# Performance work log

Measured on AMD Instinct MI355X. Metric: run time of the kernel, lower is better.

## Reference

```python
import jax, jax.numpy as jnp
import numpy as np

DIM = 256
HEADS = 8
WS = 7          # window_size
WN = 8          # window_num per side
H = W = WS * WN # 56
B = 32
MLP_HIDDEN = 4 * DIM
SCALE = (DIM // HEADS) ** -0.5
LN_EPS = 1e-5


def _rel_index(ws):
    # pairwise relative position index inside a ws x ws window (dense 0..(2ws-1)^2-1,
    # so remap_position_index is the identity relabeling)
    ch, cw = np.meshgrid(np.arange(ws), np.arange(ws), indexing='ij')
    cf = np.stack([ch.ravel(), cw.ravel()])            # (2, ws*ws)
    rel = cf[:, :, None] - cf[:, None, :]              # (2, N, N)
    rel = rel.transpose(1, 2, 0).astype(np.int32)
    rel[..., 0] += ws - 1
    rel[..., 1] += ws - 1
    rel[..., 0] *= 2 * ws - 1
    return rel.sum(-1)                                 # (N, N) in [0, (2ws-1)^2)


def _layernorm(x, g, b):
    m = x.mean(-1, keepdims=True)
    v = ((x - m) ** 2).mean(-1, keepdims=True)
    return (x - m) * jax.lax.rsqrt(v + LN_EPS) * g + b


def _mhsa(x, qkv_w, qkv_b, proj_w, proj_b, bias):
    # x: (B_, N, C); bias: (nH, N, N) or None
    B_, N, C = x.shape
    hd = C // HEADS
    qkv = (x @ qkv_w.T + qkv_b).reshape(B_, N, 3, HEADS, hd).transpose(2, 0, 3, 1, 4)
    q, k, v = qkv[0], qkv[1], qkv[2]
    attn = jnp.einsum('bhqd,bhkd->bhqk', q * SCALE, k)
    if bias is not None:
        attn = attn + bias[None]
    attn = jax.nn.softmax(attn, axis=-1)
    out = jnp.einsum('bhqk,bhkd->bhqd', attn, v).transpose(0, 2, 1, 3).reshape(B_, N, C)
    return out @ proj_w.T + proj_b


def setup_inputs() -> dict:
    key = jax.random.key(0)
    ks = jax.random.split(key, 8)
    f32 = jnp.float32
    return {
        'regional_tokens': jax.random.normal(ks[0], (B, WN * WN, DIM), f32),
        'x': jax.random.normal(ks[1], (B, H * W, DIM), f32),
        'norm1_g': jnp.ones((DIM,), f32), 'norm1_b': jnp.zeros((DIM,), f32),
        'norm2_g': jnp.ones((DIM,), f32), 'norm2_b': jnp.zeros((DIM,), f32),
        'norm3_g': jnp.ones((DIM,), f32), 'norm3_b': jnp.zeros((DIM,), f32),
        'qkv_w': jax.random.normal(ks[2], (3 * DIM, DIM), f32) * 0.02,
        'qkv_b': jnp.zeros((3 * DIM,), f32),
        'proj_w': jax.random.normal(ks[3], (DIM, DIM), f32) * 0.02,
        'proj_b': jnp.zeros((DIM,), f32),
        'bias_table': jax.random.normal(ks[4], ((2 * WS - 1) ** 2, HEADS), f32) * 0.02,
        'fc1_w': jax.random.normal(ks[5], (MLP_HIDDEN, DIM), f32) * 0.02,
        'fc1_b': jnp.zeros((MLP_HIDDEN,), f32),
        'fc2_w': jax.random.normal(ks[6], (DIM, MLP_HIDDEN), f32) * 0.02,
        'fc2_b': jnp.zeros((DIM,), f32),
        'rel_index': jnp.asarray(_rel_index(WS)),
    }


def reference(regional_tokens, x, norm1_g, norm1_b, norm2_g, norm2_b, norm3_g, norm3_b,
              qkv_w, qkv_b, proj_w, proj_b, bias_table, fc1_w, fc1_b, fc2_w, fc2_b,
              rel_index):
    Bb, L, C = x.shape
    nW = regional_tokens.shape[1]
    ws2 = WS * WS
    # --- RSA: attention over regional tokens (no relative bias) ---
    regional_tokens = regional_tokens + _mhsa(
        _layernorm(regional_tokens, norm1_g, norm1_b), qkv_w, qkv_b, proj_w, proj_b, None)
    # --- window partition of x: (B,H,W,C) -> (nW*B, ws*ws, C) (batch-major) ---
    xw = x.reshape(Bb, H // WS, WS, W // WS, WS, C)
    xw = xw.transpose(0, 1, 3, 2, 4, 5).reshape(-1, ws2, C)
    # regional tokens reshaped window-major, exactly as the torch code does
    reg = regional_tokens.transpose(1, 0, 2).reshape(nW * Bb, 1, C)
    t = jnp.concatenate([reg, xw], axis=1)  # (nW*B, 1+ws2, C)
    # --- LSA relative position bias, zero-padded for the regional token ---
    bias = bias_table[rel_index]                       # (ws2, ws2, nH)
    bias = jnp.pad(bias, ((1, 0), (1, 0), (0, 0)))      # (1+ws2, 1+ws2, nH)
    bias = bias.transpose(2, 0, 1)                      # (nH, N, N)
    t = t + _mhsa(_layernorm(t, norm2_g, norm2_b), qkv_w, qkv_b, proj_w, proj_b, bias)
    # --- MLP ---
    h = _layernorm(t, norm3_g, norm3_b)
    h = jax.nn.gelu(h @ fc1_w.T + fc1_b, approximate=False) @ fc2_w.T + fc2_b
    t = t + h
    # --- split back ---
    reg_out = t[:, 0, :].reshape(nW, Bb, C).transpose(1, 0, 2)   # (B, nW, C)
    xw = t[:, 1:, :].reshape(Bb, H // WS, W // WS, WS, WS, C)
    x_out = xw.transpose(0, 1, 3, 2, 4, 5).reshape(Bb, L, C)
    return reg_out, x_out
```

## Files before the change

kernel.cpp:

```cpp
#include <hip/hip_runtime.h>
#include <math.h>

#define SCALE_Q 0.17677669529663687f

typedef __attribute__((ext_vector_type(8))) short bf16x8;
typedef __attribute__((ext_vector_type(4))) float f32x4;
typedef __attribute__((ext_vector_type(4))) unsigned short u16x4;

static __device__ __forceinline__ unsigned short f2bf(float f) {
    unsigned int u = __float_as_uint(f);
    u += 0x7FFF + ((u >> 16) & 1);
    return (unsigned short)(u >> 16);
}

static __device__ __forceinline__ float gelu_fast(float v) {
    float s = v * (0.7978845608f + 0.0356774081f * v * v);
    float e = __expf(-2.0f * s);
    return v * __builtin_amdgcn_rcpf(1.0f + e);
}

static __device__ __forceinline__ void barrier_lds_only() {
    asm volatile("s_waitcnt lgkmcnt(0)" ::: "memory");
    __builtin_amdgcn_s_barrier();
    asm volatile("" ::: "memory");
}

__global__ void prep_kernel(const float* __restrict__ qkv_w, const float* __restrict__ proj_w,
                            const float* __restrict__ fc1_w, const float* __restrict__ fc2_w,
                            const float* __restrict__ bias_table, const int* __restrict__ rel_index,
                            unsigned short* __restrict__ wq, unsigned short* __restrict__ wp,
                            unsigned short* __restrict__ w1, unsigned short* __restrict__ w2,
                            float* __restrict__ bias_pad) {
    int tid = blockIdx.x * blockDim.x + threadIdx.x;
    int stride = gridDim.x * blockDim.x;
    for (int i = tid; i < 768 * 256; i += stride) wq[i] = f2bf(qkv_w[i]);
    for (int i = tid; i < 256 * 256; i += stride) wp[i] = f2bf(proj_w[i]);
    for (int i = tid; i < 1024 * 256; i += stride) w1[i] = f2bf(fc1_w[i]);
    for (int i = tid; i < 256 * 1024; i += stride) w2[i] = f2bf(fc2_w[i]);
    for (int i = tid; i < 8 * 64 * 64; i += stride) {
        int h = i >> 12, q = (i >> 6) & 63, k = i & 63;
        float v;
        if (k >= 50) v = -1e30f;
        else if (q == 0 || k == 0 || q >= 50) v = 0.f;
        else v = bias_table[rel_index[(q - 1) * 49 + (k - 1)] * 8 + h];
        bias_pad[i] = v;
    }
}

template <int IS_RSA>
__global__ __launch_bounds__(1024, 4) void attn_kernel(
    const float* __restrict__ reg_tok, const float* __restrict__ x,
    const float* __restrict__ reg2_in, float* __restrict__ out,
    const float* __restrict__ ln_g, const float* __restrict__ ln_b,
    const unsigned short* __restrict__ wq, const float* __restrict__ qkv_b,
    const unsigned short* __restrict__ wp, const float* __restrict__ proj_b,
    const float* __restrict__ bias_pad) {
    __shared__ __align__(16) unsigned char smem[140288];
    unsigned short* regA = (unsigned short*)smem;
    unsigned short* regB = (unsigned short*)(smem + 36864);
    unsigned short* vT   = (unsigned short*)(smem + 103424);

    const int tid = threadIdx.x;
    const int lane = tid & 63;
    const int wid = tid >> 6;
    const int widu = __builtin_amdgcn_readfirstlane(wid);
    const int l15 = lane & 15;
    const int lg = lane >> 4;
    const int u = blockIdx.x;
    const int NV = IS_RSA ? 64 : 50;
    const f32x4 fzero = {0.f, 0.f, 0.f, 0.f};

    int reg_off = 0, xb = 0, wi = 0, wj = 0;
    if (!IS_RSA) {
        reg_off = ((u & 31) * 64 + (u >> 5)) * 256;
        xb = u >> 6;
        int xn = u & 63;
        wi = xn >> 3; wj = xn & 7;
    }

    for (int r = wid; r < 64; r += 16) {
        if (r < NV) {
            const float* src;
            if (IS_RSA) src = reg_tok + (u * 64 + r) * 256;
            else if (r == 0) src = reg2_in + reg_off;
            else {
                int p = r - 1;
                src = x + (xb * 3136 + (wi * 7 + p / 7) * 56 + (wj * 7 + p % 7)) * 256;
            }
            f32x4 v = *(const f32x4*)(src + lane * 4);
            float s = v[0] + v[1] + v[2] + v[3];
            float s2 = v[0] * v[0] + v[1] * v[1] + v[2] * v[2] + v[3] * v[3];
            #pragma unroll
            for (int m = 1; m < 64; m <<= 1) { s += __shfl_xor(s, m); s2 += __shfl_xor(s2, m); }
            float mean = s * 0.00390625f;
            float rstd = rsqrtf(s2 * 0.00390625f - mean * mean + 1e-5f);
            u16x4 o;
            #pragma unroll
            for (int j = 0; j < 4; ++j) {
                int c = lane * 4 + j;
                o[j] = f2bf((v[j] - mean) * rstd * ln_g[c] + ln_b[c]);
            }
            *(u16x4*)(regA + r * 264 + lane * 4) = o;
        } else {
            u16x4 z = {0, 0, 0, 0};
            *(u16x4*)(regA + r * 264 + lane * 4) = z;
        }
    }
    barrier_lds_only();

    const int h = wid >> 1;
    const int qb = (wid & 1) * 32;

    bf16x8 wpf[8];
    {
        f32x4 acc[4][3];
        #pragma unroll
        for (int mi = 0; mi < 4; ++mi)
            #pragma unroll
            for (int t = 0; t < 3; ++t) acc[mi][t] = fzero;
        #pragma unroll
        for (int ks = 0; ks < 8; ++ks) {
            int k = ks * 32 + lg * 8;
            bf16x8 a[4], b[3];
            #pragma unroll
            for (int mi = 0; mi < 4; ++mi) a[mi] = *(const bf16x8*)(regA + (mi * 16 + l15) * 264 + k);
            #pragma unroll
            for (int t = 0; t < 3; ++t) b[t] = *(const bf16x8*)(wq + (wid * 48 + t * 16 + l15) * 256 + k);
            #pragma unroll
            for (int mi = 0; mi < 4; ++mi)
                #pragma unroll
                for (int t = 0; t < 3; ++t)
                    acc[mi][t] = __builtin_amdgcn_mfma_f32_16x16x32_bf16(a[mi], b[t], acc[mi][t], 0, 0, 0);
        }
        #pragma unroll
        for (int ks = 0; ks < 8; ++ks)
            wpf[ks] = *(const bf16x8*)(wp + (wid * 16 + l15) * 256 + ks * 32 + lg * 8);
        #pragma unroll
        for (int t = 0; t < 3; ++t) {
            if (3 * widu + t < 32) {
                #pragma unroll
                for (int mi = 0; mi < 4; ++mi) {
                    int col = wid * 48 + t * 16 + l15;
                    float bias = qkv_b[col];
                    #pragma unroll
                    for (int r = 0; r < 4; ++r) {
                        int row = mi * 16 + lg * 4 + r;
                        regB[row * 520 + col] = f2bf(acc[mi][t][r] + bias);
                    }
                }
            } else {
                #pragma unroll
                for (int mi = 0; mi < 4; ++mi) {
                    int col = wid * 48 + t * 16 + l15;
                    float bias = qkv_b[col];
                    #pragma unroll
                    for (int r = 0; r < 4; ++r) {
                        int row = mi * 16 + lg * 4 + r;
                        vT[(col - 512) * 72 + row] = f2bf(acc[mi][t][r] + bias);
                    }
                }
            }
        }
    }

    f32x4 bv[4][2];
    if (!IS_RSA) {
        #pragma unroll
        for (int mi = 0; mi < 4; ++mi)
            #pragma unroll
            for (int nj = 0; nj < 2; ++nj)
                bv[mi][nj] = *(const f32x4*)(bias_pad + h * 4096 + (qb + nj * 16 + l15) * 64 + mi * 16 + lg * 4);
    }
    barrier_lds_only();

    f32x4 st[4][2];
    {
        int k0 = h * 32 + lg * 8;
        bf16x8 af[4], bfq[2];
        #pragma unroll
        for (int mi = 0; mi < 4; ++mi) af[mi] = *(const bf16x8*)(regB + (mi * 16 + l15) * 520 + 256 + k0);
        #pragma unroll
        for (int nj = 0; nj < 2; ++nj) bfq[nj] = *(const bf16x8*)(regB + (qb + nj * 16 + l15) * 520 + k0);
        #pragma unroll
        for (int mi = 0; mi < 4; ++mi)
            #pragma unroll
            for (int nj = 0; nj < 2; ++nj)
                st[mi][nj] = __builtin_amdgcn_mfma_f32_16x16x32_bf16(af[mi], bfq[nj], fzero, 0, 0, 0);
    }

    u16x4 pf[4][2];
    #pragma unroll
    for (int nj = 0; nj < 2; ++nj) {
        float ps[4][4];
        float mx = -3.0e38f;
        #pragma unroll
        for (int mi = 0; mi < 4; ++mi)
            #pragma unroll
            for (int r = 0; r < 4; ++r) {
                float t = st[mi][nj][r] * SCALE_Q;
                if (!IS_RSA) t += bv[mi][nj][r];
                ps[mi][r] = t;
                mx = fmaxf(mx, t);
            }
        mx = fmaxf(mx, __shfl_xor(mx, 16));
        mx = fmaxf(mx, __shfl_xor(mx, 32));
        float sum = 0.f;
        #pragma unroll
        for (int mi = 0; mi < 4; ++mi)
            #pragma unroll
            for (int r = 0; r < 4; ++r) { ps[mi][r] = __expf(ps[mi][r] - mx); sum += ps[mi][r]; }
        sum += __shfl_xor(sum, 16);
        sum += __shfl_xor(sum, 32);
        float inv = __builtin_amdgcn_rcpf(sum);
        #pragma unroll
        for (int mi = 0; mi < 4; ++mi) {
            u16x4 p4;
            #pragma unroll
            for (int r = 0; r < 4; ++r) p4[r] = f2bf(ps[mi][r] * inv);
            pf[mi][nj] = p4;
        }
    }

    f32x4 ov[2][2];
    #pragma unroll
    for (int m2 = 0; m2 < 2; ++m2) { ov[m2][0] = fzero; ov[m2][1] = fzero; }
    #pragma unroll
    for (int kt = 0; kt < 4; ++kt) {
        bf16x8 pb[2];
        #pragma unroll
        for (int nj = 0; nj < 2; ++nj) {
            bf16x8 t;
            t[0] = (short)pf[kt][nj][0]; t[1] = (short)pf[kt][nj][1];
            t[2] = (short)pf[kt][nj][2]; t[3] = (short)pf[kt][nj][3];
            t[4] = 0; t[5] = 0; t[6] = 0; t[7] = 0;
            pb[nj] = t;
        }
        #pragma unroll
        for (int m2 = 0; m2 < 2; ++m2) {
            u16x4 av = *(const u16x4*)(vT + (h * 32 + m2 * 16 + l15) * 72 + kt * 16 + lg * 4);
            bf16x8 a8;
            a8[0] = (short)av[0]; a8[1] = (short)av[1]; a8[2] = (short)av[2]; a8[3] = (short)av[3];
            a8[4] = 0; a8[5] = 0; a8[6] = 0; a8[7] = 0;
            #pragma unroll
            for (int nj = 0; nj < 2; ++nj)
                ov[m2][nj] = __builtin_amdgcn_mfma_f32_16x16x32_bf16(a8, pb[nj], ov[m2][nj], 0, 0, 0);
        }
    }
    #pragma unroll
    for (int m2 = 0; m2 < 2; ++m2)
        #pragma unroll
        for (int nj = 0; nj < 2; ++nj) {
            u16x4 o4;
            #pragma unroll
            for (int r = 0; r < 4; ++r) o4[r] = f2bf(ov[m2][nj][r]);
            *(u16x4*)(regA + (qb + nj * 16 + l15) * 264 + h * 32 + m2 * 16 + lg * 4) = o4;
        }
    barrier_lds_only();

    {
        f32x4 acc[4];
        #pragma unroll
        for (int mi = 0; mi < 4; ++mi) acc[mi] = fzero;
        #pragma unroll
        for (int ks = 0; ks < 8; ++ks) {
            int k = ks * 32 + lg * 8;
            bf16x8 a[4];
            #pragma unroll
            for (int mi = 0; mi < 4; ++mi) a[mi] = *(const bf16x8*)(regA + (mi * 16 + l15) * 264 + k);
            #pragma unroll
            for (int mi = 0; mi < 4; ++mi)
                acc[mi] = __builtin_amdgcn_mfma_f32_16x16x32_bf16(a[mi], wpf[ks], acc[mi], 0, 0, 0);
        }
        int col = wid * 16 + l15;
        float pb = proj_b[col];
        #pragma unroll
        for (int mi = 0; mi < 4; ++mi)
            #pragma unroll
            for (int r = 0; r < 4; ++r) {
                int row = mi * 16 + lg * 4 + r;
                if (row < NV) {
                    float val = acc[mi][r] + pb;
                    if (IS_RSA) {
                        int off = (u * 64 + row) * 256 + col;
                        out[off] = val + reg_tok[off];
                    } else if (row == 0) {
                        out[reg_off + col] = val + reg2_in[reg_off + col];
                    } else {
                        int p = row - 1;
                        int off = (xb * 3136 + (wi * 7 + p / 7) * 56 + (wj * 7 + p % 7)) * 256 + col;
                        out[524288 + off] = val + x[off];
                    }
                }
            }
    }
}

__global__ __launch_bounds__(512, 4) void mlp_kernel(
    float* __restrict__ dout,
    const float* __restrict__ ln_g, const float* __restrict__ ln_b,
    const unsigned short* __restrict__ w1, const float* __restrict__ b1,
    const unsigned short* __restrict__ w2, const float* __restrict__ b2) {
    __shared__ __align__(16) unsigned short xst[64 * 264];
    __shared__ __align__(16) unsigned short hld[2][64 * 136];
    const int tid = threadIdx.x;
    const int lane = tid & 63;
    const int wid = tid >> 6;
    const int l15 = lane & 15;
    const int lg = lane >> 4;
    const int row0 = blockIdx.x * 64;
    const f32x4 fzero = {0.f, 0.f, 0.f, 0.f};

    #pragma unroll
    for (int i = 0; i < 8; ++i) {
        int r = wid * 8 + i;
        f32x4 v = *(const f32x4*)(dout + (row0 + r) * 256 + lane * 4);
        float s = v[0] + v[1] + v[2] + v[3];
        float s2 = v[0] * v[0] + v[1] * v[1] + v[2] * v[2] + v[3] * v[3];
        #pragma unroll
        for (int m = 1; m < 64; m <<= 1) { s += __shfl_xor(s, m); s2 += __shfl_xor(s2, m); }
        float mean = s * 0.00390625f;
        float rstd = rsqrtf(s2 * 0.00390625f - mean * mean + 1e-5f);
        u16x4 o;
        #pragma unroll
        for (int j = 0; j < 4; ++j) {
            int c = lane * 4 + j;
            o[j] = f2bf((v[j] - mean) * rstd * ln_g[c] + ln_b[c]);
        }
        *(u16x4*)(xst + r * 264 + lane * 4) = o;
    }

    bf16x8 w1f[8];
    #pragma unroll
    for (int ks = 0; ks < 8; ++ks)
        w1f[ks] = *(const bf16x8*)(w1 + (wid * 16 + l15) * 256 + ks * 32 + lg * 8);
    barrier_lds_only();

    f32x4 acc2[4][2];
    #pragma unroll
    for (int mi = 0; mi < 4; ++mi) { acc2[mi][0] = fzero; acc2[mi][1] = fzero; }

    #pragma unroll
    for (int c = 0; c < 8; ++c) {
        unsigned short* hb = &hld[c & 1][0];
        f32x4 acc1[4];
        #pragma unroll
        for (int mi = 0; mi < 4; ++mi) acc1[mi] = fzero;
        #pragma unroll
        for (int ks = 0; ks < 8; ++ks) {
            int k = ks * 32 + lg * 8;
            bf16x8 a[4];
            #pragma unroll
            for (int mi = 0; mi < 4; ++mi)
                a[mi] = *(const bf16x8*)(xst + (mi * 16 + l15) * 264 + k);
            #pragma unroll
            for (int mi = 0; mi < 4; ++mi)
                acc1[mi] = __builtin_amdgcn_mfma_f32_16x16x32_bf16(a[mi], w1f[ks], acc1[mi], 0, 0, 0);
        }
        if (c < 7) {
            #pragma unroll
            for (int ks = 0; ks < 8; ++ks)
                w1f[ks] = *(const bf16x8*)(w1 + ((c + 1) * 128 + wid * 16 + l15) * 256 + ks * 32 + lg * 8);
        }
        {
            int hc = wid * 16 + l15;
            float bb = b1[c * 128 + hc];
            #pragma unroll
            for (int mi = 0; mi < 4; ++mi)
                #pragma unroll
                for (int r = 0; r < 4; ++r)
                    hb[(mi * 16 + lg * 4 + r) * 136 + hc] = f2bf(gelu_fast(acc1[mi][r] + bb));
        }
        bf16x8 w2f[8];
        #pragma unroll
        for (int ks = 0; ks < 4; ++ks)
            #pragma unroll
            for (int ni = 0; ni < 2; ++ni)
                w2f[ks * 2 + ni] = *(const bf16x8*)(w2 + (wid * 32 + ni * 16 + l15) * 1024 + c * 128 + ks * 32 + lg * 8);
        barrier_lds_only();
        #pragma unroll
        for (int ks = 0; ks < 4; ++ks) {
            int k = ks * 32 + lg * 8;
            bf16x8 a[4];
            #pragma unroll
            for (int mi = 0; mi < 4; ++mi)
                a[mi] = *(const bf16x8*)(hb + (mi * 16 + l15) * 136 + k);
            #pragma unroll
            for (int mi = 0; mi < 4; ++mi)
                #pragma unroll
                for (int ni = 0; ni < 2; ++ni)
                    acc2[mi][ni] = __builtin_amdgcn_mfma_f32_16x16x32_bf16(a[mi], w2f[ks * 2 + ni], acc2[mi][ni], 0, 0, 0);
        }
    }
    #pragma unroll
    for (int mi = 0; mi < 4; ++mi)
        #pragma unroll
        for (int ni = 0; ni < 2; ++ni) {
            int col = wid * 32 + ni * 16 + l15;
            float bb = b2[col];
            #pragma unroll
            for (int r = 0; r < 4; ++r) {
                int row = row0 + mi * 16 + lg * 4 + r;
                float* dst = dout + row * 256 + col;
                *dst = acc2[mi][ni][r] + bb + *dst;
            }
        }
}

extern "C" void kernel_launch(void* const* d_in, const int* in_sizes, int n_in,
                              void* d_out, int out_size, void* d_ws, size_t ws_size,
                              hipStream_t stream) {
    const float* regional = (const float*)d_in[0];
    const float* x = (const float*)d_in[1];
    const float* n1g = (const float*)d_in[2];
    const float* n1b = (const float*)d_in[3];
    const float* n2g = (const float*)d_in[4];
    const float* n2b = (const float*)d_in[5];
    const float* n3g = (const float*)d_in[6];
    const float* n3b = (const float*)d_in[7];
    const float* qkvw = (const float*)d_in[8];
    const float* qkvb = (const float*)d_in[9];
    const float* projw = (const float*)d_in[10];
    const float* projb = (const float*)d_in[11];
    const float* btab = (const float*)d_in[12];
    const float* f1w = (const float*)d_in[13];
    const float* f1b = (const float*)d_in[14];
    const float* f2w = (const float*)d_in[15];
    const float* f2b = (const float*)d_in[16];
    const int* relidx = (const int*)d_in[17];

    unsigned char* ws = (unsigned char*)d_ws;
    unsigned short* wq = (unsigned short*)(ws);
    unsigned short* wp = (unsigned short*)(ws + 393216);
    unsigned short* w1 = (unsigned short*)(ws + 524288);
    unsigned short* w2 = (unsigned short*)(ws + 1048576);
    float* bias_pad    = (float*)(ws + 1572864);
    float* reg2        = (float*)(ws + 1703936);

    float* out = (float*)d_out;

    prep_kernel<<<512, 256, 0, stream>>>(qkvw, projw, f1w, f2w, btab, relidx, wq, wp, w1, w2, bias_pad);
    attn_kernel<1><<<32, 1024, 0, stream>>>(regional, x, nullptr, reg2, n1g, n1b, wq, qkvb, wp, projb, nullptr);
    attn_kernel<0><<<2048, 1024, 0, stream>>>(regional, x, reg2, out, n2g, n2b, wq, qkvb, wp, projb, bias_pad);
    mlp_kernel<<<1600, 512, 0, stream>>>(out, n3g, n3b, w1, f1b, w2, f2b);
}
```

Measured before the change: 498.4 us.

## Split fused MLP into separate FC1 and FC2 kernels over row chunks

Replaces the single fused MLP kernel, which kept the hidden activation in LDS, with an FC1+GELU kernel that writes a bf16 hidden buffer to workspace and an FC2 kernel that reads it back and adds the residual. The work runs in four row chunks so the hidden buffer stays small and may stay cache-resident. The aim is better MFMA tiling and occupancy in each GEMM, paid for with extra global traffic for the hidden tensor, eight launches instead of one, and LayerNorm being recomputed for each of the two column halves.

```diff
diff --git a/kernel.cpp b/kernel.cpp
--- a/kernel.cpp
+++ b/kernel.cpp
@@ -295,13 +295,11 @@
     }
 }
 
-__global__ __launch_bounds__(512, 4) void mlp_kernel(
-    float* __restrict__ dout,
-    const float* __restrict__ ln_g, const float* __restrict__ ln_b,
-    const unsigned short* __restrict__ w1, const float* __restrict__ b1,
-    const unsigned short* __restrict__ w2, const float* __restrict__ b2) {
+__global__ __launch_bounds__(512, 4) void fc1_kernel(
+    const float* __restrict__ tin, const float* __restrict__ ln_g,
+    const float* __restrict__ ln_b, const unsigned short* __restrict__ w1,
+    const float* __restrict__ b1, unsigned short* __restrict__ H) {
     __shared__ __align__(16) unsigned short xst[64 * 264];
-    __shared__ __align__(16) unsigned short hld[2][64 * 136];
     const int tid = threadIdx.x;
     const int lane = tid & 63;
     const int wid = tid >> 6;
@@ -313,7 +311,7 @@
     #pragma unroll
     for (int i = 0; i < 8; ++i) {
         int r = wid * 8 + i;
-        f32x4 v = *(const f32x4*)(dout + (row0 + r) * 256 + lane * 4);
+        f32x4 v = *(const f32x4*)(tin + (row0 + r) * 256 + lane * 4);
         float s = v[0] + v[1] + v[2] + v[3];
         float s2 = v[0] * v[0] + v[1] * v[1] + v[2] * v[2] + v[3] * v[3];
         #pragma unroll
@@ -328,82 +326,82 @@
         }
         *(u16x4*)(xst + r * 264 + lane * 4) = o;
     }
-
-    bf16x8 w1f[8];
-    #pragma unroll
-    for (int ks = 0; ks < 8; ++ks)
-        w1f[ks] = *(const bf16x8*)(w1 + (wid * 16 + l15) * 256 + ks * 32 + lg * 8);
-    barrier_lds_only();
-
-    f32x4 acc2[4][2];
-    #pragma unroll
-    for (int mi = 0; mi < 4; ++mi) { acc2[mi][0] = fzero; acc2[mi][1] = fzero; }
-
-    #pragma unroll
-    for (int c = 0; c < 8; ++c) {
-        unsigned short* hb = &hld[c & 1][0];
-        f32x4 acc1[4];
-        #pragma unroll
-        for (int mi = 0; mi < 4; ++mi) acc1[mi] = fzero;
-        #pragma unroll
-        for (int ks = 0; ks < 8; ++ks) {
-            int k = ks * 32 + lg * 8;
-            bf16x8 a[4];
-            #pragma unroll
-            for (int mi = 0; mi < 4; ++mi)
-                a[mi] = *(const bf16x8*)(xst + (mi * 16 + l15) * 264 + k);
-            #pragma unroll
-            for (int mi = 0; mi < 4; ++mi)
-                acc1[mi] = __builtin_amdgcn_mfma_f32_16x16x32_bf16(a[mi], w1f[ks], acc1[mi], 0, 0, 0);
-        }
-        if (c < 7) {
-            #pragma unroll
-            for (int ks = 0; ks < 8; ++ks)
-                w1f[ks] = *(const bf16x8*)(w1 + ((c + 1) * 128 + wid * 16 + l15) * 256 + ks * 32 + lg * 8);
-        }
-        {
-            int hc = wid * 16 + l15;
-            float bb = b1[c * 128 + hc];
-            #pragma unroll
-            for (int mi = 0; mi < 4; ++mi)
-                #pragma unroll
-                for (int r = 0; r < 4; ++r)
-                    hb[(mi * 16 + lg * 4 + r) * 136 + hc] = f2bf(gelu_fast(acc1[mi][r] + bb));
-        }
-        bf16x8 w2f[8];
-        #pragma unroll
-        for (int ks = 0; ks < 4; ++ks)
-            #pragma unroll
-            for (int ni = 0; ni < 2; ++ni)
-                w2f[ks * 2 + ni] = *(const bf16x8*)(w2 + (wid * 32 + ni * 16 + l15) * 1024 + c * 128 + ks * 32 + lg * 8);
-        barrier_lds_only();
-        #pragma unroll
-        for (int ks = 0; ks < 4; ++ks) {
-            int k = ks * 32 + lg * 8;
-            bf16x8 a[4];
-            #pragma unroll
-            for (int mi = 0; mi < 4; ++mi)
-                a[mi] = *(const bf16x8*)(hb + (mi * 16 + l15) * 136 + k);
-            #pragma unroll
-            for (int mi = 0; mi < 4; ++mi)
-                #pragma unroll
-                for (int ni = 0; ni < 2; ++ni)
-                    acc2[mi][ni] = __builtin_amdgcn_mfma_f32_16x16x32_bf16(a[mi], w2f[ks * 2 + ni], acc2[mi][ni], 0, 0, 0);
-        }
-    }
+    __syncthreads();
+
+    const int colbase = blockIdx.y * 512 + wid * 64;
+    f32x4 acc[4][4];
     #pragma unroll
     for (int mi = 0; mi < 4; ++mi)
         #pragma unroll
-        for (int ni = 0; ni < 2; ++ni) {
-            int col = wid * 32 + ni * 16 + l15;
-            float bb = b2[col];
+        for (int ni = 0; ni < 4; ++ni) acc[mi][ni] = fzero;
+    #pragma unroll
+    for (int ks = 0; ks < 8; ++ks) {
+        int k = ks * 32 + lg * 8;
+        bf16x8 a[4], b[4];
+        #pragma unroll
+        for (int mi = 0; mi < 4; ++mi)
+            a[mi] = *(const bf16x8*)(xst + (mi * 16 + l15) * 264 + k);
+        #pragma unroll
+        for (int ni = 0; ni < 4; ++ni)
+            b[ni] = *(const bf16x8*)(w1 + (colbase + ni * 16 + l15) * 256 + k);
+        #pragma unroll
+        for (int mi = 0; mi < 4; ++mi)
+            #pragma unroll
+            for (int ni = 0; ni < 4; ++ni)
+                acc[mi][ni] = __builtin_amdgcn_mfma_f32_16x16x32_bf16(a[mi], b[ni], acc[mi][ni], 0, 0, 0);
+    }
+    #pragma unroll
+    for (int mi = 0; mi < 4; ++mi)
+        #pragma unroll
+        for (int ni = 0; ni < 4; ++ni) {
+            int col = colbase + ni * 16 + l15;
+            float bb = b1[col];
             #pragma unroll
             for (int r = 0; r < 4; ++r) {
                 int row = row0 + mi * 16 + lg * 4 + r;
-                float* dst = dout + row * 256 + col;
-                *dst = acc2[mi][ni][r] + bb + *dst;
-            }
-        }
+                H[row * 1024 + col] = f2bf(gelu_fast(acc[mi][ni][r] + bb));
+            }
+        }
+}
+
+__global__ __launch_bounds__(512, 6) void fc2_kernel(
+    const unsigned short* __restrict__ H, const unsigned short* __restrict__ w2,
+    const float* __restrict__ b2, float* __restrict__ dout) {
+    const int tid = threadIdx.x;
+    const int lane = tid & 63;
+    const int wid = tid >> 6;
+    const int l15 = lane & 15;
+    const int lg = lane >> 4;
+    const int wr = wid >> 1;
+    const int wc = wid & 1;
+    const int rowb = blockIdx.x * 64 + wr * 16;
+    const int colb = blockIdx.y * 128 + wc * 64;
+    const f32x4 fzero = {0.f, 0.f, 0.f, 0.f};
+
+    f32x4 acc[4];
+    #pragma unroll
+    for (int ni = 0; ni < 4; ++ni) acc[ni] = fzero;
+    #pragma unroll
+    for (int ks = 0; ks < 32; ++ks) {
+        int k = ks * 32 + lg * 8;
+        bf16x8 a = *(const bf16x8*)(H + (rowb + l15) * 1024 + k);
+        #pragma unroll
+        for (int ni = 0; ni < 4; ++ni) {
+            bf16x8 b = *(const bf16x8*)(w2 + (colb + ni * 16 + l15) * 1024 + k);
+            acc[ni] = __builtin_amdgcn_mfma_f32_16x16x32_bf16(a, b, acc[ni], 0, 0, 0);
+        }
+    }
+    #pragma unroll
+    for (int ni = 0; ni < 4; ++ni) {
+        int col = colb + ni * 16 + l15;
+        float bb = b2[col];
+        #pragma unroll
+        for (int r = 0; r < 4; ++r) {
+            int row = rowb + lg * 4 + r;
+            float* dst = dout + row * 256 + col;
+            *dst = acc[ni][r] + bb + *dst;
+        }
+    }
 }
 
 extern "C" void kernel_launch(void* const* d_in, const int* in_sizes, int n_in,
@@ -435,11 +433,16 @@
     unsigned short* w2 = (unsigned short*)(ws + 1048576);
     float* bias_pad    = (float*)(ws + 1572864);
     float* reg2        = (float*)(ws + 1703936);
+    unsigned short* Hb = (unsigned short*)(ws + 3801088);
 
     float* out = (float*)d_out;
 
     prep_kernel<<<512, 256, 0, stream>>>(qkvw, projw, f1w, f2w, btab, relidx, wq, wp, w1, w2, bias_pad);
     attn_kernel<1><<<32, 1024, 0, stream>>>(regional, x, nullptr, reg2, n1g, n1b, wq, qkvb, wp, projb, nullptr);
     attn_kernel<0><<<2048, 1024, 0, stream>>>(regional, x, reg2, out, n2g, n2b, wq, qkvb, wp, projb, bias_pad);
-    mlp_kernel<<<1600, 512, 0, stream>>>(out, n3g, n3b, w1, f1b, w2, f2b);
-}
+    for (int c = 0; c < 4; ++c) {
+        float* tc = out + (size_t)c * 25600 * 256;
+        fc1_kernel<<<dim3(400, 2), 512, 0, stream>>>(tc, n3g, n3b, w1, f1b, Hb);
+        fc2_kernel<<<dim3(400, 2), 512, 0, stream>>>(Hb, w2, f2b, tc);
+    }
+}
```

After: 1.040 ms. 2.09x slower.

## Restructure attention kernel to one head per wave with register-resident Q/K/V

Applied to the files above, without the earlier changes.

The attention kernel moves from 1024 threads (two waves per head, each owning half the queries) to 512 threads with one wave per head covering all 64 queries. Each wave computes its own K, Q and V head slices with MFMA and keeps them in registers as zero-padded bf16 fragments, so the large LDS staging buffers for QKV and the transposed V go away. LDS per block shrinks to a single 64x264 bf16 tile, which should allow more resident blocks and cut LDS traffic. In exchange there are fewer waves per block, more registers per wave, and the projection weights are now streamed from global memory inside the k loop instead of being preloaded.

```diff
diff --git a/kernel.cpp b/kernel.cpp
--- a/kernel.cpp
+++ b/kernel.cpp
@@ -48,26 +48,23 @@
 }
 
 template <int IS_RSA>
-__global__ __launch_bounds__(1024, 4) void attn_kernel(
+__global__ __launch_bounds__(512, 4) void attn_kernel(
     const float* __restrict__ reg_tok, const float* __restrict__ x,
     const float* __restrict__ reg2_in, float* __restrict__ out,
     const float* __restrict__ ln_g, const float* __restrict__ ln_b,
     const unsigned short* __restrict__ wq, const float* __restrict__ qkv_b,
     const unsigned short* __restrict__ wp, const float* __restrict__ proj_b,
     const float* __restrict__ bias_pad) {
-    __shared__ __align__(16) unsigned char smem[140288];
-    unsigned short* regA = (unsigned short*)smem;
-    unsigned short* regB = (unsigned short*)(smem + 36864);
-    unsigned short* vT   = (unsigned short*)(smem + 103424);
+    __shared__ __align__(16) unsigned short xln[64 * 264];
 
     const int tid = threadIdx.x;
     const int lane = tid & 63;
     const int wid = tid >> 6;
-    const int widu = __builtin_amdgcn_readfirstlane(wid);
     const int l15 = lane & 15;
     const int lg = lane >> 4;
     const int u = blockIdx.x;
     const int NV = IS_RSA ? 64 : 50;
+    const int h = wid;
     const f32x4 fzero = {0.f, 0.f, 0.f, 0.f};
 
     int reg_off = 0, xb = 0, wi = 0, wj = 0;
@@ -78,7 +75,9 @@
         wi = xn >> 3; wj = xn & 7;
     }
 
-    for (int r = wid; r < 64; r += 16) {
+    #pragma unroll
+    for (int i = 0; i < 8; ++i) {
+        int r = i * 8 + wid;
         if (r < NV) {
             const float* src;
             if (IS_RSA) src = reg_tok + (u * 64 + r) * 256;
@@ -100,108 +99,99 @@
                 int c = lane * 4 + j;
                 o[j] = f2bf((v[j] - mean) * rstd * ln_g[c] + ln_b[c]);
             }
-            *(u16x4*)(regA + r * 264 + lane * 4) = o;
+            *(u16x4*)(xln + r * 264 + lane * 4) = o;
         } else {
             u16x4 z = {0, 0, 0, 0};
-            *(u16x4*)(regA + r * 264 + lane * 4) = z;
-        }
-    }
-    barrier_lds_only();
-
-    const int h = wid >> 1;
-    const int qb = (wid & 1) * 32;
-
-    bf16x8 wpf[8];
+            *(u16x4*)(xln + r * 264 + lane * 4) = z;
+        }
+    }
+    __syncthreads();
+
+    bf16x8 a16k[2][4];
     {
-        f32x4 acc[4][3];
+        f32x4 Kc[2][4];
+        #pragma unroll
+        for (int dc = 0; dc < 2; ++dc)
+            #pragma unroll
+            for (int nt = 0; nt < 4; ++nt) Kc[dc][nt] = fzero;
+        #pragma unroll
+        for (int ks = 0; ks < 8; ++ks) {
+            int k = ks * 32 + lg * 8;
+            bf16x8 aw[2], bx[4];
+            #pragma unroll
+            for (int dc = 0; dc < 2; ++dc)
+                aw[dc] = *(const bf16x8*)(wq + (256 + h * 32 + dc * 16 + l15) * 256 + k);
+            #pragma unroll
+            for (int nt = 0; nt < 4; ++nt)
+                bx[nt] = *(const bf16x8*)(xln + (nt * 16 + l15) * 264 + k);
+            #pragma unroll
+            for (int dc = 0; dc < 2; ++dc)
+                #pragma unroll
+                for (int nt = 0; nt < 4; ++nt)
+                    Kc[dc][nt] = __builtin_amdgcn_mfma_f32_16x16x32_bf16(aw[dc], bx[nt], Kc[dc][nt], 0, 0, 0);
+        }
+        #pragma unroll
+        for (int dc = 0; dc < 2; ++dc) {
+            f32x4 bk = *(const f32x4*)(qkv_b + 256 + h * 32 + dc * 16 + lg * 4);
+            #pragma unroll
+            for (int nt = 0; nt < 4; ++nt) {
+                bf16x8 t;
+                #pragma unroll
+                for (int j = 0; j < 4; ++j) t[j] = (short)f2bf(Kc[dc][nt][j] + bk[j]);
+                t[4] = 0; t[5] = 0; t[6] = 0; t[7] = 0;
+                a16k[dc][nt] = t;
+            }
+        }
+    }
+
+    u16x4 pf[4][4];
+    #pragma unroll
+    for (int nj = 0; nj < 4; ++nj) {
+        f32x4 Qc[2] = {fzero, fzero};
+        #pragma unroll
+        for (int ks = 0; ks < 8; ++ks) {
+            int k = ks * 32 + lg * 8;
+            bf16x8 aw[2];
+            #pragma unroll
+            for (int dc = 0; dc < 2; ++dc)
+                aw[dc] = *(const bf16x8*)(wq + (h * 32 + dc * 16 + l15) * 256 + k);
+            bf16x8 bq = *(const bf16x8*)(xln + (nj * 16 + l15) * 264 + k);
+            #pragma unroll
+            for (int dc = 0; dc < 2; ++dc)
+                Qc[dc] = __builtin_amdgcn_mfma_f32_16x16x32_bf16(aw[dc], bq, Qc[dc], 0, 0, 0);
+        }
+        bf16x8 b16[2];
+        #pragma unroll
+        for (int dc = 0; dc < 2; ++dc) {
+            f32x4 bq = *(const f32x4*)(qkv_b + h * 32 + dc * 16 + lg * 4);
+            bf16x8 t;
+            #pragma unroll
+            for (int j = 0; j < 4; ++j) t[j] = (short)f2bf(Qc[dc][j] + bq[j]);
+            t[4] = 0; t[5] = 0; t[6] = 0; t[7] = 0;
+            b16[dc] = t;
+        }
+        f32x4 st[4];
+        #pragma unroll
+        for (int mi = 0; mi < 4; ++mi) st[mi] = fzero;
         #pragma unroll
         for (int mi = 0; mi < 4; ++mi)
             #pragma unroll
-            for (int t = 0; t < 3; ++t) acc[mi][t] = fzero;
-        #pragma unroll
-        for (int ks = 0; ks < 8; ++ks) {
-            int k = ks * 32 + lg * 8;
-            bf16x8 a[4], b[3];
-            #pragma unroll
-            for (int mi = 0; mi < 4; ++mi) a[mi] = *(const bf16x8*)(regA + (mi * 16 + l15) * 264 + k);
-            #pragma unroll
-            for (int t = 0; t < 3; ++t) b[t] = *(const bf16x8*)(wq + (wid * 48 + t * 16 + l15) * 256 + k);
-            #pragma unroll
-            for (int mi = 0; mi < 4; ++mi)
-                #pragma unroll
-                for (int t = 0; t < 3; ++t)
-                    acc[mi][t] = __builtin_amdgcn_mfma_f32_16x16x32_bf16(a[mi], b[t], acc[mi][t], 0, 0, 0);
-        }
-        #pragma unroll
-        for (int ks = 0; ks < 8; ++ks)
-            wpf[ks] = *(const bf16x8*)(wp + (wid * 16 + l15) * 256 + ks * 32 + lg * 8);
-        #pragma unroll
-        for (int t = 0; t < 3; ++t) {
-            if (3 * widu + t < 32) {
-                #pragma unroll
-                for (int mi = 0; mi < 4; ++mi) {
-                    int col = wid * 48 + t * 16 + l15;
-                    float bias = qkv_b[col];
-                    #pragma unroll
-                    for (int r = 0; r < 4; ++r) {
-                        int row = mi * 16 + lg * 4 + r;
-                        regB[row * 520 + col] = f2bf(acc[mi][t][r] + bias);
-                    }
-                }
-            } else {
-                #pragma unroll
-                for (int mi = 0; mi < 4; ++mi) {
-                    int col = wid * 48 + t * 16 + l15;
-                    float bias = qkv_b[col];
-                    #pragma unroll
-                    for (int r = 0; r < 4; ++r) {
-                        int row = mi * 16 + lg * 4 + r;
-                        vT[(col - 512) * 72 + row] = f2bf(acc[mi][t][r] + bias);
-                    }
-                }
-            }
-        }
-    }
-
-    f32x4 bv[4][2];
-    if (!IS_RSA) {
-        #pragma unroll
-        for (int mi = 0; mi < 4; ++mi)
-            #pragma unroll
-            for (int nj = 0; nj < 2; ++nj)
-                bv[mi][nj] = *(const f32x4*)(bias_pad + h * 4096 + (qb + nj * 16 + l15) * 64 + mi * 16 + lg * 4);
-    }
-    barrier_lds_only();
-
-    f32x4 st[4][2];
-    {
-        int k0 = h * 32 + lg * 8;
-        bf16x8 af[4], bfq[2];
-        #pragma unroll
-        for (int mi = 0; mi < 4; ++mi) af[mi] = *(const bf16x8*)(regB + (mi * 16 + l15) * 520 + 256 + k0);
-        #pragma unroll
-        for (int nj = 0; nj < 2; ++nj) bfq[nj] = *(const bf16x8*)(regB + (qb + nj * 16 + l15) * 520 + k0);
-        #pragma unroll
-        for (int mi = 0; mi < 4; ++mi)
-            #pragma unroll
-            for (int nj = 0; nj < 2; ++nj)
-                st[mi][nj] = __builtin_amdgcn_mfma_f32_16x16x32_bf16(af[mi], bfq[nj], fzero, 0, 0, 0);
-    }
-
-    u16x4 pf[4][2];
-    #pragma unroll
-    for (int nj = 0; nj < 2; ++nj) {
+            for (int dc = 0; dc < 2; ++dc)
+                st[mi] = __builtin_amdgcn_mfma_f32_16x16x32_bf16(a16k[dc][mi], b16[dc], st[mi], 0, 0, 0);
         float ps[4][4];
         float mx = -3.0e38f;
         #pragma unroll
-        for (int mi = 0; mi < 4; ++mi)
+        for (int mi = 0; mi < 4; ++mi) {
+            f32x4 bv = fzero;
+            if (!IS_RSA)
+                bv = *(const f32x4*)(bias_pad + h * 4096 + (nj * 16 + l15) * 64 + mi * 16 + lg * 4);
             #pragma unroll
             for (int r = 0; r < 4; ++r) {
-                float t = st[mi][nj][r] * SCALE_Q;
-                if (!IS_RSA) t += bv[mi][nj][r];
+                float t = st[mi][r] * SCALE_Q + bv[r];
                 ps[mi][r] = t;
                 mx = fmaxf(mx, t);
             }
+        }
         mx = fmaxf(mx, __shfl_xor(mx, 16));
         mx = fmaxf(mx, __shfl_xor(mx, 32));
         float sum = 0.f;
@@ -221,14 +211,52 @@
         }
     }
 
-    f32x4 ov[2][2];
-    #pragma unroll
-    for (int m2 = 0; m2 < 2; ++m2) { ov[m2][0] = fzero; ov[m2][1] = fzero; }
+    bf16x8 a8[4][2];
+    {
+        f32x4 Vc[4][2];
+        #pragma unroll
+        for (int mt = 0; mt < 4; ++mt) { Vc[mt][0] = fzero; Vc[mt][1] = fzero; }
+        #pragma unroll
+        for (int ks = 0; ks < 8; ++ks) {
+            int k = ks * 32 + lg * 8;
+            bf16x8 ax[4], bw[2];
+            #pragma unroll
+            for (int mt = 0; mt < 4; ++mt)
+                ax[mt] = *(const bf16x8*)(xln + (mt * 16 + l15) * 264 + k);
+            #pragma unroll
+            for (int nt = 0; nt < 2; ++nt)
+                bw[nt] = *(const bf16x8*)(wq + (512 + h * 32 + nt * 16 + l15) * 256 + k);
+            #pragma unroll
+            for (int mt = 0; mt < 4; ++mt)
+                #pragma unroll
+                for (int nt = 0; nt < 2; ++nt)
+                    Vc[mt][nt] = __builtin_amdgcn_mfma_f32_16x16x32_bf16(ax[mt], bw[nt], Vc[mt][nt], 0, 0, 0);
+        }
+        float bv0 = qkv_b[512 + h * 32 + l15];
+        float bv1 = qkv_b[512 + h * 32 + 16 + l15];
+        #pragma unroll
+        for (int kt = 0; kt < 4; ++kt)
+            #pragma unroll
+            for (int m2 = 0; m2 < 2; ++m2) {
+                float bb = m2 ? bv1 : bv0;
+                bf16x8 t;
+                #pragma unroll
+                for (int j = 0; j < 4; ++j) t[j] = (short)f2bf(Vc[kt][m2][j] + bb);
+                t[4] = 0; t[5] = 0; t[6] = 0; t[7] = 0;
+                a8[kt][m2] = t;
+            }
+    }
+
+    f32x4 ov[2][4];
+    #pragma unroll
+    for (int m2 = 0; m2 < 2; ++m2)
+        #pragma unroll
+        for (int nj = 0; nj < 4; ++nj) ov[m2][nj] = fzero;
     #pragma unroll
     for (int kt = 0; kt < 4; ++kt) {
-        bf16x8 pb[2];
-        #pragma unroll
-        for (int nj = 0; nj < 2; ++nj) {
+        bf16x8 pb[4];
+        #pragma unroll
+        for (int nj = 0; nj < 4; ++nj) {
             bf16x8 t;
             t[0] = (short)pf[kt][nj][0]; t[1] = (short)pf[kt][nj][1];
             t[2] = (short)pf[kt][nj][2]; t[3] = (short)pf[kt][nj][3];
@@ -236,62 +264,69 @@
             pb[nj] = t;
         }
         #pragma unroll
-        for (int m2 = 0; m2 < 2; ++m2) {
-            u16x4 av = *(const u16x4*)(vT + (h * 32 + m2 * 16 + l15) * 72 + kt * 16 + lg * 4);
-            bf16x8 a8;
-            a8[0] = (short)av[0]; a8[1] = (short)av[1]; a8[2] = (short)av[2]; a8[3] = (short)av[3];
-            a8[4] = 0; a8[5] = 0; a8[6] = 0; a8[7] = 0;
-            #pragma unroll
-            for (int nj = 0; nj < 2; ++nj)
-                ov[m2][nj] = __builtin_amdgcn_mfma_f32_16x16x32_bf16(a8, pb[nj], ov[m2][nj], 0, 0, 0);
-        }
-    }
+        for (int m2 = 0; m2 < 2; ++m2)
+            #pragma unroll
+            for (int nj = 0; nj < 4; ++nj)
+                ov[m2][nj] = __builtin_amdgcn_mfma_f32_16x16x32_bf16(a8[kt][m2], pb[nj], ov[m2][nj], 0, 0, 0);
+    }
+    __syncthreads();
+
     #pragma unroll
     for (int m2 = 0; m2 < 2; ++m2)
         #pragma unroll
-        for (int nj = 0; nj < 2; ++nj) {
+        for (int nj = 0; nj < 4; ++nj) {
             u16x4 o4;
             #pragma unroll
             for (int r = 0; r < 4; ++r) o4[r] = f2bf(ov[m2][nj][r]);
-            *(u16x4*)(regA + (qb + nj * 16 + l15) * 264 + h * 32 + m2 * 16 + lg * 4) = o4;
-        }
-    barrier_lds_only();
+            *(u16x4*)(xln + (nj * 16 + l15) * 264 + h * 32 + m2 * 16 + lg * 4) = o4;
+        }
+    __syncthreads();
 
     {
-        f32x4 acc[4];
-        #pragma unroll
-        for (int mi = 0; mi < 4; ++mi) acc[mi] = fzero;
+        int nb = wid * 32;
+        f32x4 acc[4][2];
+        #pragma unroll
+        for (int mi = 0; mi < 4; ++mi) { acc[mi][0] = fzero; acc[mi][1] = fzero; }
         #pragma unroll
         for (int ks = 0; ks < 8; ++ks) {
             int k = ks * 32 + lg * 8;
-            bf16x8 a[4];
-            #pragma unroll
-            for (int mi = 0; mi < 4; ++mi) a[mi] = *(const bf16x8*)(regA + (mi * 16 + l15) * 264 + k);
-            #pragma unroll
-            for (int mi = 0; mi < 4; ++mi)
-                acc[mi] = __builtin_amdgcn_mfma_f32_16x16x32_bf16(a[mi], wpf[ks], acc[mi], 0, 0, 0);
-        }
-        int col = wid * 16 + l15;
-        float pb = proj_b[col];
-        #pragma unroll
-        for (int mi = 0; mi < 4; ++mi)
-            #pragma unroll
-            for (int r = 0; r < 4; ++r) {
-                int row = mi * 16 + lg * 4 + r;
-                if (row < NV) {
-                    float val = acc[mi][r] + pb;
-                    if (IS_RSA) {
-                        int off = (u * 64 + row) * 256 + col;
-                        out[off] = val + reg_tok[off];
-                    } else if (row == 0) {
-                        out[reg_off + col] = val + reg2_in[reg_off + col];
-                    } else {
-                        int p = row - 1;
-                        int off = (xb * 3136 + (wi * 7 + p / 7) * 56 + (wj * 7 + p % 7)) * 256 + col;
-                        out[524288 + off] = val + x[off];
+            bf16x8 a[4], b[2];
+            #pragma unroll
+            for (int mi = 0; mi < 4; ++mi)
+                a[mi] = *(const bf16x8*)(xln + (mi * 16 + l15) * 264 + k);
+            #pragma unroll
+            for (int t = 0; t < 2; ++t)
+                b[t] = *(const bf16x8*)(wp + (nb + t * 16 + l15) * 256 + k);
+            #pragma unroll
+            for (int mi = 0; mi < 4; ++mi)
+                #pragma unroll
+                for (int t = 0; t < 2; ++t)
+                    acc[mi][t] = __builtin_amdgcn_mfma_f32_16x16x32_bf16(a[mi], b[t], acc[mi][t], 0, 0, 0);
+        }
+        #pragma unroll
+        for (int t = 0; t < 2; ++t) {
+            int col = nb + t * 16 + l15;
+            float pb = proj_b[col];
+            #pragma unroll
+            for (int mi = 0; mi < 4; ++mi)
+                #pragma unroll
+                for (int r = 0; r < 4; ++r) {
+                    int row = mi * 16 + lg * 4 + r;
+                    if (row < NV) {
+                        float val = acc[mi][t][r] + pb;
+                        if (IS_RSA) {
+                            int off = (u * 64 + row) * 256 + col;
+                            out[off] = val + reg_tok[off];
+                        } else if (row == 0) {
+                            out[reg_off + col] = val + reg2_in[reg_off + col];
+                        } else {
+                            int p = row - 1;
+                            int off = (xb * 3136 + (wi * 7 + p / 7) * 56 + (wj * 7 + p % 7)) * 256 + col;
+                            out[524288 + off] = val + x[off];
+                        }
                     }
                 }
-            }
+        }
     }
 }
 
@@ -439,7 +474,7 @@
     float* out = (float*)d_out;
 
     prep_kernel<<<512, 256, 0, stream>>>(qkvw, projw, f1w, f2w, btab, relidx, wq, wp, w1, w2, bias_pad);
-    attn_kernel<1><<<32, 1024, 0, stream>>>(regional, x, nullptr, reg2, n1g, n1b, wq, qkvb, wp, projb, nullptr);
-    attn_kernel<0><<<2048, 1024, 0, stream>>>(regional, x, reg2, out, n2g, n2b, wq, qkvb, wp, projb, bias_pad);
+    attn_kernel<1><<<32, 512, 0, stream>>>(regional, x, nullptr, reg2, n1g, n1b, wq, qkvb, wp, projb, nullptr);
+    attn_kernel<0><<<2048, 512, 0, stream>>>(regional, x, reg2, out, n2g, n2b, wq, qkvb, wp, projb, bias_pad);
     mlp_kernel<<<1600, 512, 0, stream>>>(out, n3g, n3b, w1, f1b, w2, f2b);
 }
```

New measurement: 982.7 us. +97.2%, slower.

## Retile MLP kernel warps into 2x4 grid and drop weight register prefetch

Applied to the files above, without the earlier changes.

The MLP kernel now splits its 8 warps into a 2x4 grid over rows and columns, so each warp computes a 32-row by 32-col (fc1) or 32x64 (fc2) tile instead of all 64 rows by a narrow column strip. This halves the LDS A-fragment reads per warp. Weights are now loaded from global memory inside the k-loop rather than prefetched into registers a chunk ahead, which lowers register pressure but may expose global load latency. The attention kernel's qkv store is also restructured into a per-element column branch, replacing the wave-uniform branch.

```diff
diff --git a/kernel.cpp b/kernel.cpp
--- a/kernel.cpp
+++ b/kernel.cpp
@@ -63,7 +63,6 @@
     const int tid = threadIdx.x;
     const int lane = tid & 63;
     const int wid = tid >> 6;
-    const int widu = __builtin_amdgcn_readfirstlane(wid);
     const int l15 = lane & 15;
     const int lg = lane >> 4;
     const int u = blockIdx.x;
@@ -136,31 +135,19 @@
         for (int ks = 0; ks < 8; ++ks)
             wpf[ks] = *(const bf16x8*)(wp + (wid * 16 + l15) * 256 + ks * 32 + lg * 8);
         #pragma unroll
-        for (int t = 0; t < 3; ++t) {
-            if (3 * widu + t < 32) {
+        for (int mi = 0; mi < 4; ++mi)
+            #pragma unroll
+            for (int t = 0; t < 3; ++t) {
+                int col = wid * 48 + t * 16 + l15;
+                float bias = qkv_b[col];
                 #pragma unroll
-                for (int mi = 0; mi < 4; ++mi) {
-                    int col = wid * 48 + t * 16 + l15;
-                    float bias = qkv_b[col];
-                    #pragma unroll
-                    for (int r = 0; r < 4; ++r) {
-                        int row = mi * 16 + lg * 4 + r;
-                        regB[row * 520 + col] = f2bf(acc[mi][t][r] + bias);
-                    }
+                for (int r = 0; r < 4; ++r) {
+                    int row = mi * 16 + lg * 4 + r;
+                    unsigned short hv = f2bf(acc[mi][t][r] + bias);
+                    if (col < 512) regB[row * 520 + col] = hv;
+                    else vT[(col - 512) * 72 + row] = hv;
                 }
-            } else {
-                #pragma unroll
-                for (int mi = 0; mi < 4; ++mi) {
-                    int col = wid * 48 + t * 16 + l15;
-                    float bias = qkv_b[col];
-                    #pragma unroll
-                    for (int r = 0; r < 4; ++r) {
-                        int row = mi * 16 + lg * 4 + r;
-                        vT[(col - 512) * 72 + row] = f2bf(acc[mi][t][r] + bias);
-                    }
-                }
-            }
-        }
+            }
     }
 
     f32x4 bv[4][2];
@@ -307,6 +294,8 @@
     const int wid = tid >> 6;
     const int l15 = lane & 15;
     const int lg = lane >> 4;
+    const int wm = wid >> 2;
+    const int wn = wid & 3;
     const int row0 = blockIdx.x * 64;
     const f32x4 fzero = {0.f, 0.f, 0.f, 0.f};
 
@@ -328,78 +317,75 @@
         }
         *(u16x4*)(xst + r * 264 + lane * 4) = o;
     }
-
-    bf16x8 w1f[8];
-    #pragma unroll
-    for (int ks = 0; ks < 8; ++ks)
-        w1f[ks] = *(const bf16x8*)(w1 + (wid * 16 + l15) * 256 + ks * 32 + lg * 8);
     barrier_lds_only();
 
-    f32x4 acc2[4][2];
-    #pragma unroll
-    for (int mi = 0; mi < 4; ++mi) { acc2[mi][0] = fzero; acc2[mi][1] = fzero; }
+    f32x4 acc2[2][4];
+    #pragma unroll
+    for (int mi = 0; mi < 2; ++mi)
+        #pragma unroll
+        for (int ni = 0; ni < 4; ++ni) acc2[mi][ni] = fzero;
 
     #pragma unroll
     for (int c = 0; c < 8; ++c) {
         unsigned short* hb = &hld[c & 1][0];
-        f32x4 acc1[4];
-        #pragma unroll
-        for (int mi = 0; mi < 4; ++mi) acc1[mi] = fzero;
+        f32x4 acc1[2][2];
+        #pragma unroll
+        for (int mi = 0; mi < 2; ++mi) { acc1[mi][0] = fzero; acc1[mi][1] = fzero; }
         #pragma unroll
         for (int ks = 0; ks < 8; ++ks) {
             int k = ks * 32 + lg * 8;
-            bf16x8 a[4];
-            #pragma unroll
-            for (int mi = 0; mi < 4; ++mi)
-                a[mi] = *(const bf16x8*)(xst + (mi * 16 + l15) * 264 + k);
-            #pragma unroll
-            for (int mi = 0; mi < 4; ++mi)
-                acc1[mi] = __builtin_amdgcn_mfma_f32_16x16x32_bf16(a[mi], w1f[ks], acc1[mi], 0, 0, 0);
-        }
-        if (c < 7) {
-            #pragma unroll
-            for (int ks = 0; ks < 8; ++ks)
-                w1f[ks] = *(const bf16x8*)(w1 + ((c + 1) * 128 + wid * 16 + l15) * 256 + ks * 32 + lg * 8);
-        }
-        {
-            int hc = wid * 16 + l15;
-            float bb = b1[c * 128 + hc];
-            #pragma unroll
-            for (int mi = 0; mi < 4; ++mi)
+            bf16x8 a[2], b[2];
+            #pragma unroll
+            for (int mi = 0; mi < 2; ++mi)
+                a[mi] = *(const bf16x8*)(xst + (wm * 32 + mi * 16 + l15) * 264 + k);
+            #pragma unroll
+            for (int ni = 0; ni < 2; ++ni)
+                b[ni] = *(const bf16x8*)(w1 + (c * 128 + wn * 32 + ni * 16 + l15) * 256 + k);
+            #pragma unroll
+            for (int mi = 0; mi < 2; ++mi)
                 #pragma unroll
-                for (int r = 0; r < 4; ++r)
-                    hb[(mi * 16 + lg * 4 + r) * 136 + hc] = f2bf(gelu_fast(acc1[mi][r] + bb));
-        }
-        bf16x8 w2f[8];
-        #pragma unroll
-        for (int ks = 0; ks < 4; ++ks)
-            #pragma unroll
-            for (int ni = 0; ni < 2; ++ni)
-                w2f[ks * 2 + ni] = *(const bf16x8*)(w2 + (wid * 32 + ni * 16 + l15) * 1024 + c * 128 + ks * 32 + lg * 8);
+                for (int ni = 0; ni < 2; ++ni)
+                    acc1[mi][ni] = __builtin_amdgcn_mfma_f32_16x16x32_bf16(a[mi], b[ni], acc1[mi][ni], 0, 0, 0);
+        }
+        #pragma unroll
+        for (int mi = 0; mi < 2; ++mi)
+            #pragma unroll
+            for (int ni = 0; ni < 2; ++ni) {
+                int hc = wn * 32 + ni * 16 + l15;
+                float bb = b1[c * 128 + hc];
+                #pragma unroll
+                for (int r = 0; r < 4; ++r) {
+                    int row = wm * 32 + mi * 16 + lg * 4 + r;
+                    hb[row * 136 + hc] = f2bf(gelu_fast(acc1[mi][ni][r] + bb));
+                }
+            }
         barrier_lds_only();
         #pragma unroll
         for (int ks = 0; ks < 4; ++ks) {
             int k = ks * 32 + lg * 8;
-            bf16x8 a[4];
-            #pragma unroll
-            for (int mi = 0; mi < 4; ++mi)
-                a[mi] = *(const bf16x8*)(hb + (mi * 16 + l15) * 136 + k);
-            #pragma unroll
-            for (int mi = 0; mi < 4; ++mi)
+            bf16x8 a[2], b[4];
+            #pragma unroll
+            for (int mi = 0; mi < 2; ++mi)
+                a[mi] = *(const bf16x8*)(hb + (wm * 32 + mi * 16 + l15) * 136 + k);
+            #pragma unroll
+            for (int ni = 0; ni < 4; ++ni)
+                b[ni] = *(const bf16x8*)(w2 + (wn * 64 + ni * 16 + l15) * 1024 + c * 128 + k);
+            #pragma unroll
+            for (int mi = 0; mi < 2; ++mi)
                 #pragma unroll
-                for (int ni = 0; ni < 2; ++ni)
-                    acc2[mi][ni] = __builtin_amdgcn_mfma_f32_16x16x32_bf16(a[mi], w2f[ks * 2 + ni], acc2[mi][ni], 0, 0, 0);
-        }
-    }
-    #pragma unroll
-    for (int mi = 0; mi < 4; ++mi)
-        #pragma unroll
-        for (int ni = 0; ni < 2; ++ni) {
-            int col = wid * 32 + ni * 16 + l15;
+                for (int ni = 0; ni < 4; ++ni)
+                    acc2[mi][ni] = __builtin_amdgcn_mfma_f32_16x16x32_bf16(a[mi], b[ni], acc2[mi][ni], 0, 0, 0);
+        }
+    }
+    #pragma unroll
+    for (int mi = 0; mi < 2; ++mi)
+        #pragma unroll
+        for (int ni = 0; ni < 4; ++ni) {
+            int col = wn * 64 + ni * 16 + l15;
             float bb = b2[col];
             #pragma unroll
             for (int r = 0; r < 4; ++r) {
-                int row = row0 + mi * 16 + lg * 4 + r;
+                int row = row0 + wm * 32 + mi * 16 + lg * 4 + r;
                 float* dst = dout + row * 256 + col;
                 *dst = acc2[mi][ni][r] + bb + *dst;
             }
```

Measured after the change: 698.3 us. 1.4x slower.
